# Kernel tuning notes

Hardware: AMD Instinct MI355X
Metric: run time of the kernel (lower is better)

## Reference

```python
import jax, jax.numpy as jnp
import numpy as np

DN = ('NCDHW', 'OIDHW', 'NCDHW')  # conv dimension numbers for 3D conv in torch layout
EPS = 1e-14


def setup_inputs() -> dict:
    key = jax.random.key(0)
    k1, k2 = jax.random.split(key)
    # xs: [B, C, D, H, W]
    xs = jax.random.normal(k1, (16, 128, 24, 24, 24), dtype=jnp.float32)
    # feature_vectors (prototypes): [num_features, C, w_1, h_1, L_1]
    feature_vectors = jax.random.normal(k2, (128, 128, 3, 3, 3), dtype=jnp.float32)
    return {"xs": xs, "feature_vectors": feature_vectors}


def reference(xs, feature_vectors):
    F_, C, kd, kh, kw = feature_vectors.shape
    # ||x_patch||^2: the original convolves xs**2 with all-ones weights of shape
    # [F, C, kd, kh, kw], producing F identical channels. We compute a single
    # sum-pool channel (same math) and let broadcasting supply the F channels.
    ones = jnp.ones((1, C, kd, kh, kw), dtype=xs.dtype)
    xs_squared_l2 = jax.lax.conv_general_dilated(
        xs * xs, ones, window_strides=(1, 1, 1), padding='VALID',
        dimension_numbers=DN)  # [B, 1, D', H', W']
    # ||p||^2 per prototype: [F, 1, 1, 1]
    ps_squared_l2 = jnp.sum(feature_vectors * feature_vectors,
                            axis=(1, 2, 3, 4)).reshape(-1, 1, 1, 1)
    # <x_patch, p>: the real weighted conv. [B, F, D', H', W']
    xs_conv = jax.lax.conv_general_dilated(
        xs, feature_vectors, window_strides=(1, 1, 1), padding='VALID',
        dimension_numbers=DN)
    distance = xs_squared_l2 + ps_squared_l2 - 2.0 * xs_conv
    return jnp.sqrt(jnp.abs(distance) + EPS)
```

## Files before the change

### kernel.cpp

```cpp
#include <hip/hip_runtime.h>
#include <hip/hip_bf16.h>

typedef __attribute__((ext_vector_type(8))) __bf16 bf16x8;
typedef __attribute__((ext_vector_type(2))) __bf16 bf16x2;
typedef __attribute__((ext_vector_type(4))) float f32x4;

#define B_   16
#define C_   128
#define DIM  24
#define F_   128
#define OD   22
#define OS   (OD*OD*OD)
#define SPB  (DIM*DIM*DIM)
#define K_   3456
#define M_   (B_*OS)
#define OUTN (B_*F_*OS)

__device__ __forceinline__ void async16(const void* g, void* l) {
  __builtin_amdgcn_global_load_lds(
      (const __attribute__((address_space(1))) unsigned int*)g,
      (__attribute__((address_space(3))) unsigned int*)l, 16, 0, 0);
}

__global__ __launch_bounds__(256) void prep_x(const float* __restrict__ xs,
                                              __bf16* __restrict__ xt,
                                              float* __restrict__ s1) {
  __shared__ float tile[C_ * 97];
  __shared__ float red[192];
  const int blk = blockIdx.x;
  const int yg = blk % 6;
  const int t2 = blk / 6;
  const int z = t2 % DIM;
  const int b = t2 / DIM;
  const int t = threadIdx.x;
  const float* src = xs + (size_t)b * C_ * SPB + z * (DIM * DIM) + yg * 96;
  for (int it = 0; it < 12; ++it) {
    int idx = it * 256 + t;
    int c = idx / 24, f4 = idx - c * 24;
    const float4 v = *(const float4*)(src + (size_t)c * SPB + f4 * 4);
    float* d = &tile[c * 97 + f4 * 4];
    d[0] = v.x; d[1] = v.y; d[2] = v.z; d[3] = v.w;
  }
  __syncthreads();
  size_t obase = ((size_t)b * SPB + z * (DIM * DIM) + yg * 96) * C_;
  for (int it = 0; it < 24; ++it) {
    int idx = it * 256 + t;
    int c2 = idx & 63, x = idx >> 6;
    bf16x2 v;
    v[0] = (__bf16)tile[(2 * c2) * 97 + x];
    v[1] = (__bf16)tile[(2 * c2 + 1) * 97 + x];
    *(bf16x2*)&xt[obase + (size_t)x * C_ + 2 * c2] = v;
  }
  if (t < 192) {
    int g = t / 96, p = t - g * 96;
    float s = 0.f;
    for (int c = g; c < C_; c += 2) {
      float v = tile[c * 97 + p];
      s += v * v;
    }
    red[g * 96 + p] = s;
  }
  __syncthreads();
  if (t < 96)
    s1[((size_t)b * SPB + z * (DIM * DIM) + yg * 96) + t] = red[t] + red[96 + t];
}

__global__ void prep_w(const float* __restrict__ fv, __bf16* __restrict__ Wt,
                       float* __restrict__ psq) {
  __shared__ float tile[K_];
  const int f = blockIdx.x;
  const float* src = fv + (size_t)f * K_;
  float part = 0.f;
  for (int idx = threadIdx.x; idx < K_; idx += 256) {
    float v = src[idx];
    tile[idx] = v;
    part += v * v;
  }
  __syncthreads();
  for (int idx = threadIdx.x; idx < K_; idx += 256) {
    int c = idx & 127, off = idx >> 7;
    Wt[(size_t)f * K_ + idx] = (__bf16)tile[c * 27 + off];
  }
  for (int o = 32; o > 0; o >>= 1) part += __shfl_down(part, o, 64);
  __shared__ float red[4];
  int w = threadIdx.x >> 6, l = threadIdx.x & 63;
  if (l == 0) red[w] = part;
  __syncthreads();
  if (threadIdx.x == 0) psq[f] = red[0] + red[1] + red[2] + red[3];
}

__global__ void pool_sq(const float* __restrict__ s1, float* __restrict__ xsq) {
  int i = blockIdx.x * 256 + threadIdx.x;
  if (i >= M_) return;
  int ow = i % OD;
  int t = i / OD;
  int oh = t % OD; t /= OD;
  int od = t % OD;
  int b = t / OD;
  const float* p = s1 + ((b * DIM + od) * DIM + oh) * DIM + ow;
  float s = 0.f;
#pragma unroll
  for (int dz = 0; dz < 3; ++dz)
#pragma unroll
    for (int dy = 0; dy < 3; ++dy)
#pragma unroll
      for (int dx = 0; dx < 3; ++dx)
        s += p[dz * 576 + dy * 24 + dx];
  xsq[i] = s;
}

__global__ __launch_bounds__(256) void l2gemm(
    const __bf16* __restrict__ xt, const __bf16* __restrict__ Wt,
    const float* __restrict__ xsq, const float* __restrict__ psq,
    float* __restrict__ out) {
  __shared__ __align__(16) __bf16 Wl[128 * 64];
  __shared__ __align__(16) __bf16 Pl[128 * 64];
  const int t = threadIdx.x;
  const int l = t & 63, w = t >> 6;
  const int quad = l >> 4, lan = l & 15;
  const int e = t & 7, r0 = t >> 3;
  const int esw = (e ^ (r0 & 7)) * 8;
  const int mt = blockIdx.x;

  int sb[4];
#pragma unroll
  for (int p = 0; p < 4; ++p) {
    int m = mt * 128 + r0 + 32 * p;
    int b = m / OS;
    int s = m - b * OS;
    int od = s / (OD * OD);
    int s2 = s - od * (OD * OD);
    int oh = s2 / OD;
    int ow = s2 - oh * OD;
    sb[p] = b * SPB + od * 576 + oh * 24 + ow;
  }

  f32x4 acc[4][4];
#pragma unroll
  for (int i = 0; i < 4; ++i)
#pragma unroll
    for (int n = 0; n < 4; ++n) acc[i][n] = (f32x4){0.f, 0.f, 0.f, 0.f};

  const int wm = (w >> 1) * 64;
  const int wn = (w & 1) * 64;
  __bf16* wl_base = &Wl[(w * 8) * 64];
  __bf16* pl_base = &Pl[(w * 8) * 64];

#pragma unroll 1
  for (int kt = 0; kt < 54; ++kt) {
    int off = kt >> 1;
    int dz = off / 9;
    int rem = off - dz * 9;
    int dy = rem / 3;
    int dx = rem - dy * 3;
    int doff = dz * 576 + dy * 24 + dx;
    int c0 = (kt & 1) << 6;
    __syncthreads();
#pragma unroll
    for (int p = 0; p < 4; ++p) {
      const __bf16* gp = xt + (((size_t)(sb[p] + doff)) << 7) + c0 + esw;
      async16(gp, pl_base + (size_t)(32 * p) * 64);
      const __bf16* gw = Wt + (size_t)(r0 + 32 * p) * K_ + kt * 64 + esw;
      async16(gw, wl_base + (size_t)(32 * p) * 64);
    }
    __syncthreads();
#pragma unroll
    for (int kk = 0; kk < 2; ++kk) {
      bf16x8 a[4], bb[4];
      const int swz = (((kk * 4 + quad) ^ (lan & 7))) * 8;
#pragma unroll
      for (int i = 0; i < 4; ++i)
        a[i] = *(const bf16x8*)&Wl[(wm + i * 16 + lan) * 64 + swz];
#pragma unroll
      for (int n = 0; n < 4; ++n)
        bb[n] = *(const bf16x8*)&Pl[(wn + n * 16 + lan) * 64 + swz];
#pragma unroll
      for (int i = 0; i < 4; ++i)
#pragma unroll
        for (int n = 0; n < 4; ++n)
          acc[i][n] = __builtin_amdgcn_mfma_f32_16x16x32_bf16(a[i], bb[n],
                                                              acc[i][n], 0, 0, 0);
    }
  }

  int mb[4];
  float xv[4];
#pragma unroll
  for (int n = 0; n < 4; ++n) {
    int m = mt * 128 + wn + n * 16 + lan;
    int b = m / OS;
    int s = m - b * OS;
    mb[n] = b * (F_ * OS) + s;
    xv[n] = xsq[m];
  }
#pragma unroll
  for (int i = 0; i < 4; ++i) {
#pragma unroll
    for (int r = 0; r < 4; ++r) {
      int f = wm + i * 16 + quad * 4 + r;
      float pq = psq[f];
#pragma unroll
      for (int n = 0; n < 4; ++n) {
        float d = xv[n] + pq - 2.0f * acc[i][n][r];
        out[mb[n] + f * OS] = sqrtf(fabsf(d) + 1e-14f);
      }
    }
  }
}

__global__ void l2conv_direct(const float* __restrict__ xs,
                              const float* __restrict__ fv,
                              float* __restrict__ out) {
  int i = blockIdx.x * 256 + threadIdx.x;
  if (i >= OUTN) return;
  int s = i % OS;
  int t2 = i / OS;
  int f = t2 & 127;
  int b = t2 >> 7;
  int od = s / (OD * OD);
  int s2 = s - od * (OD * OD);
  int oh = s2 / OD;
  int ow = s2 - oh * OD;
  const float* xp = xs + (size_t)b * C_ * SPB + od * 576 + oh * 24 + ow;
  const float* wp = fv + (size_t)f * K_;
  float dot = 0.f, xq = 0.f, pq = 0.f;
  for (int c = 0; c < C_; ++c) {
    const float* xpc = xp + (size_t)c * SPB;
    const float* wpc = wp + c * 27;
#pragma unroll
    for (int o = 0; o < 27; ++o) {
      int dz = o / 9;
      int ry = o - dz * 9;
      int dy = ry / 3;
      int dx = ry - dy * 3;
      float xv = xpc[dz * 576 + dy * 24 + dx];
      float wv = wpc[o];
      dot += xv * wv;
      xq += xv * xv;
      pq += wv * wv;
    }
  }
  out[i] = sqrtf(fabsf(xq + pq - 2.f * dot) + 1e-14f);
}

extern "C" void kernel_launch(void* const* d_in, const int* in_sizes, int n_in,
                              void* d_out, int out_size, void* d_ws,
                              size_t ws_size, hipStream_t stream) {
  const float* xs = (const float*)d_in[0];
  const float* fv = (const float*)d_in[1];
  float* out = (float*)d_out;

  const size_t xt_b  = (size_t)B_ * SPB * C_ * 2;
  const size_t wt_b  = (size_t)F_ * K_ * 2;
  const size_t s1_b  = (size_t)B_ * SPB * 4;
  const size_t xsq_b = (size_t)M_ * 4;
  const size_t psq_b = 512;
  if (ws_size < xt_b + wt_b + s1_b + xsq_b + psq_b) {
    l2conv_direct<<<(OUTN + 255) / 256, 256, 0, stream>>>(xs, fv, out);
    return;
  }
  char* p = (char*)d_ws;
  __bf16* xt = (__bf16*)p;          p += xt_b;
  __bf16* Wt = (__bf16*)p;          p += wt_b;
  float*  s1 = (float*)p;           p += s1_b;
  float*  xsq = (float*)p;          p += xsq_b;
  float*  psq = (float*)p;

  prep_x<<<B_ * DIM * DIM / 4, 256, 0, stream>>>(xs, xt, s1);
  prep_w<<<F_, 256, 0, stream>>>(fv, Wt, psq);
  pool_sq<<<(M_ + 255) / 256, 256, 0, stream>>>(s1, xsq);
  l2gemm<<<M_ / 128, 256, 0, stream>>>(xt, Wt, xsq, psq, out);
}
```

Measured before the change: 407.1 us.

## Double-buffer LDS tiles in l2gemm and remap blocks across XCDs

The GEMM main loop now uses two LDS buffers, issuing the async global-to-LDS loads for the next K tile before computing on the current one, with a single barrier per iteration instead of two. The goal is to overlap global load latency with MFMA work. Block indices are also remapped so that consecutive M tiles land on the same XCD, which should improve L2 reuse of the overlapping input patches. LDS use doubles to 64 KB per block, which may reduce occupancy. The loop waits only on __syncthreads, with no explicit vmcnt wait, so the compiler has to insert the correct waits for the async loads.

```diff
diff --git a/kernel.cpp b/kernel.cpp
--- a/kernel.cpp
+++ b/kernel.cpp
@@ -113,14 +113,19 @@
     const __bf16* __restrict__ xt, const __bf16* __restrict__ Wt,
     const float* __restrict__ xsq, const float* __restrict__ psq,
     float* __restrict__ out) {
-  __shared__ __align__(16) __bf16 Wl[128 * 64];
-  __shared__ __align__(16) __bf16 Pl[128 * 64];
+  __shared__ __align__(16) __bf16 Wl[2][128 * 64];
+  __shared__ __align__(16) __bf16 Pl[2][128 * 64];
   const int t = threadIdx.x;
   const int l = t & 63, w = t >> 6;
   const int quad = l >> 4, lan = l & 15;
   const int e = t & 7, r0 = t >> 3;
   const int esw = (e ^ (r0 & 7)) * 8;
-  const int mt = blockIdx.x;
+
+  const int nwg = gridDim.x;
+  const int orig = blockIdx.x;
+  const int xcd = orig & 7, lo = orig >> 3;
+  const int q = nwg >> 3, r = nwg & 7;
+  const int mt = (xcd < r ? xcd * (q + 1) : r * (q + 1) + (xcd - r) * q) + lo;
 
   int sb[4];
 #pragma unroll
@@ -143,11 +148,9 @@
 
   const int wm = (w >> 1) * 64;
   const int wn = (w & 1) * 64;
-  __bf16* wl_base = &Wl[(w * 8) * 64];
-  __bf16* pl_base = &Pl[(w * 8) * 64];
-
-#pragma unroll 1
-  for (int kt = 0; kt < 54; ++kt) {
+  const int wrow = w * 8;
+
+  auto stage = [&](int kt, int buf) {
     int off = kt >> 1;
     int dz = off / 9;
     int rem = off - dz * 9;
@@ -155,25 +158,35 @@
     int dx = rem - dy * 3;
     int doff = dz * 576 + dy * 24 + dx;
     int c0 = (kt & 1) << 6;
-    __syncthreads();
+    __bf16* wl = &Wl[buf][wrow * 64];
+    __bf16* pl = &Pl[buf][wrow * 64];
 #pragma unroll
     for (int p = 0; p < 4; ++p) {
       const __bf16* gp = xt + (((size_t)(sb[p] + doff)) << 7) + c0 + esw;
-      async16(gp, pl_base + (size_t)(32 * p) * 64);
+      async16(gp, pl + (size_t)(32 * p) * 64);
       const __bf16* gw = Wt + (size_t)(r0 + 32 * p) * K_ + kt * 64 + esw;
-      async16(gw, wl_base + (size_t)(32 * p) * 64);
-    }
-    __syncthreads();
+      async16(gw, wl + (size_t)(32 * p) * 64);
+    }
+  };
+
+  stage(0, 0);
+  __syncthreads();
+  int cur = 0;
+#pragma unroll 1
+  for (int kt = 0; kt < 54; ++kt) {
+    if (kt < 53) stage(kt + 1, cur ^ 1);
+    const __bf16* Wc = &Wl[cur][0];
+    const __bf16* Pc = &Pl[cur][0];
 #pragma unroll
     for (int kk = 0; kk < 2; ++kk) {
       bf16x8 a[4], bb[4];
       const int swz = (((kk * 4 + quad) ^ (lan & 7))) * 8;
 #pragma unroll
       for (int i = 0; i < 4; ++i)
-        a[i] = *(const bf16x8*)&Wl[(wm + i * 16 + lan) * 64 + swz];
+        a[i] = *(const bf16x8*)&Wc[(wm + i * 16 + lan) * 64 + swz];
 #pragma unroll
       for (int n = 0; n < 4; ++n)
-        bb[n] = *(const bf16x8*)&Pl[(wn + n * 16 + lan) * 64 + swz];
+        bb[n] = *(const bf16x8*)&Pc[(wn + n * 16 + lan) * 64 + swz];
 #pragma unroll
       for (int i = 0; i < 4; ++i)
 #pragma unroll
@@ -181,6 +194,8 @@
           acc[i][n] = __builtin_amdgcn_mfma_f32_16x16x32_bf16(a[i], bb[n],
                                                               acc[i][n], 0, 0, 0);
     }
+    __syncthreads();
+    cur ^= 1;
   }
 
   int mb[4];
@@ -196,12 +211,12 @@
 #pragma unroll
   for (int i = 0; i < 4; ++i) {
 #pragma unroll
-    for (int r = 0; r < 4; ++r) {
-      int f = wm + i * 16 + quad * 4 + r;
+    for (int r2 = 0; r2 < 4; ++r2) {
+      int f = wm + i * 16 + quad * 4 + r2;
       float pq = psq[f];
 #pragma unroll
       for (int n = 0; n < 4; ++n) {
-        float d = xv[n] + pq - 2.0f * acc[i][n][r];
+        float d = xv[n] + pq - 2.0f * acc[i][n][r2];
         out[mb[n] + f * OS] = sqrtf(fabsf(d) + 1e-14f);
       }
     }
```

Result: faster. 382.7 us (-6.0%).

## Enlarge GEMM M-tile to 256, remap blocks per XCD, raise MFMA priority

Applied to the files above, without the earlier changes.

The im2col GEMM now computes a 128x256 output tile per block, so each loaded weight tile is reused across twice as many patch rows. Each wave accumulates a 64x128 sub-tile in 32 accumulators, with bounds clamping for the partial last tile. Block indices are remapped so consecutive M-tiles land on the same XCD for L2 locality, and s_setprio raises wave priority around the MFMA bursts. The syncs are restructured to one before compute and one after. The cost is much higher register pressure under launch_bounds(256,2), more LDS per block, and fewer blocks in the grid.

```diff
diff --git a/kernel.cpp b/kernel.cpp
--- a/kernel.cpp
+++ b/kernel.cpp
@@ -109,23 +109,29 @@
   xsq[i] = s;
 }
 
-__global__ __launch_bounds__(256) void l2gemm(
+__global__ __launch_bounds__(256, 2) void l2gemm(
     const __bf16* __restrict__ xt, const __bf16* __restrict__ Wt,
     const float* __restrict__ xsq, const float* __restrict__ psq,
     float* __restrict__ out) {
   __shared__ __align__(16) __bf16 Wl[128 * 64];
-  __shared__ __align__(16) __bf16 Pl[128 * 64];
+  __shared__ __align__(16) __bf16 Pl[256 * 64];
   const int t = threadIdx.x;
   const int l = t & 63, w = t >> 6;
   const int quad = l >> 4, lan = l & 15;
   const int e = t & 7, r0 = t >> 3;
   const int esw = (e ^ (r0 & 7)) * 8;
-  const int mt = blockIdx.x;
-
-  int sb[4];
-#pragma unroll
-  for (int p = 0; p < 4; ++p) {
-    int m = mt * 128 + r0 + 32 * p;
+
+  const int nwg = gridDim.x;
+  const int orig = blockIdx.x;
+  const int xcd = orig & 7, lo = orig >> 3;
+  const int q = nwg >> 3, r = nwg & 7;
+  const int mt = (xcd < r ? xcd * (q + 1) : r * (q + 1) + (xcd - r) * q) + lo;
+
+  int sb[8];
+#pragma unroll
+  for (int p = 0; p < 8; ++p) {
+    int m = mt * 256 + r0 + 32 * p;
+    if (m >= M_) m = M_ - 1;
     int b = m / OS;
     int s = m - b * OS;
     int od = s / (OD * OD);
@@ -135,59 +141,66 @@
     sb[p] = b * SPB + od * 576 + oh * 24 + ow;
   }
 
-  f32x4 acc[4][4];
+  f32x4 acc[4][8];
 #pragma unroll
   for (int i = 0; i < 4; ++i)
 #pragma unroll
-    for (int n = 0; n < 4; ++n) acc[i][n] = (f32x4){0.f, 0.f, 0.f, 0.f};
-
-  const int wm = (w >> 1) * 64;
-  const int wn = (w & 1) * 64;
-  __bf16* wl_base = &Wl[(w * 8) * 64];
-  __bf16* pl_base = &Pl[(w * 8) * 64];
+    for (int n = 0; n < 8; ++n) acc[i][n] = (f32x4){0.f, 0.f, 0.f, 0.f};
+
+  const int wm = (w & 1) * 64;
+  const int wn = (w >> 1) * 128;
 
 #pragma unroll 1
   for (int kt = 0; kt < 54; ++kt) {
-    int off = kt >> 1;
-    int dz = off / 9;
-    int rem = off - dz * 9;
-    int dy = rem / 3;
-    int dx = rem - dy * 3;
-    int doff = dz * 576 + dy * 24 + dx;
-    int c0 = (kt & 1) << 6;
+    {
+      int off = kt >> 1;
+      int dz = off / 9;
+      int rem = off - dz * 9;
+      int dy = rem / 3;
+      int dx = rem - dy * 3;
+      int doff = dz * 576 + dy * 24 + dx;
+      int c0 = (kt & 1) << 6;
+#pragma unroll
+      for (int p = 0; p < 4; ++p) {
+        const __bf16* gw = Wt + (size_t)(r0 + 32 * p) * K_ + kt * 64 + esw;
+        async16(gw, &Wl[(size_t)(8 * w + 32 * p) * 64]);
+      }
+#pragma unroll
+      for (int p = 0; p < 8; ++p) {
+        const __bf16* gp = xt + (((size_t)(sb[p] + doff)) << 7) + c0 + esw;
+        async16(gp, &Pl[(size_t)(8 * w + 32 * p) * 64]);
+      }
+    }
     __syncthreads();
 #pragma unroll
-    for (int p = 0; p < 4; ++p) {
-      const __bf16* gp = xt + (((size_t)(sb[p] + doff)) << 7) + c0 + esw;
-      async16(gp, pl_base + (size_t)(32 * p) * 64);
-      const __bf16* gw = Wt + (size_t)(r0 + 32 * p) * K_ + kt * 64 + esw;
-      async16(gw, wl_base + (size_t)(32 * p) * 64);
-    }
-    __syncthreads();
-#pragma unroll
     for (int kk = 0; kk < 2; ++kk) {
-      bf16x8 a[4], bb[4];
-      const int swz = (((kk * 4 + quad) ^ (lan & 7))) * 8;
+      const int swz = ((kk * 4 + quad) ^ (lan & 7)) * 8;
+      bf16x8 a[4], bb[8];
 #pragma unroll
       for (int i = 0; i < 4; ++i)
         a[i] = *(const bf16x8*)&Wl[(wm + i * 16 + lan) * 64 + swz];
 #pragma unroll
-      for (int n = 0; n < 4; ++n)
+      for (int n = 0; n < 8; ++n)
         bb[n] = *(const bf16x8*)&Pl[(wn + n * 16 + lan) * 64 + swz];
+      __builtin_amdgcn_s_setprio(1);
 #pragma unroll
       for (int i = 0; i < 4; ++i)
 #pragma unroll
-        for (int n = 0; n < 4; ++n)
+        for (int n = 0; n < 8; ++n)
           acc[i][n] = __builtin_amdgcn_mfma_f32_16x16x32_bf16(a[i], bb[n],
                                                               acc[i][n], 0, 0, 0);
-    }
-  }
-
-  int mb[4];
-  float xv[4];
-#pragma unroll
-  for (int n = 0; n < 4; ++n) {
-    int m = mt * 128 + wn + n * 16 + lan;
+      __builtin_amdgcn_s_setprio(0);
+    }
+    __syncthreads();
+  }
+
+  int mb[8], mok[8];
+  float xv[8];
+#pragma unroll
+  for (int n = 0; n < 8; ++n) {
+    int m = mt * 256 + wn + n * 16 + lan;
+    mok[n] = (m < M_);
+    if (m >= M_) m = M_ - 1;
     int b = m / OS;
     int s = m - b * OS;
     mb[n] = b * (F_ * OS) + s;
@@ -196,13 +209,15 @@
 #pragma unroll
   for (int i = 0; i < 4; ++i) {
 #pragma unroll
-    for (int r = 0; r < 4; ++r) {
-      int f = wm + i * 16 + quad * 4 + r;
+    for (int r2 = 0; r2 < 4; ++r2) {
+      int f = wm + i * 16 + quad * 4 + r2;
       float pq = psq[f];
 #pragma unroll
-      for (int n = 0; n < 4; ++n) {
-        float d = xv[n] + pq - 2.0f * acc[i][n][r];
-        out[mb[n] + f * OS] = sqrtf(fabsf(d) + 1e-14f);
+      for (int n = 0; n < 8; ++n) {
+        if (mok[n]) {
+          float d = xv[n] + pq - 2.0f * acc[i][n][r2];
+          out[mb[n] + f * OS] = sqrtf(fabsf(d) + 1e-14f);
+        }
       }
     }
   }
@@ -269,5 +284,5 @@
   prep_x<<<B_ * DIM * DIM / 4, 256, 0, stream>>>(xs, xt, s1);
   prep_w<<<F_, 256, 0, stream>>>(fv, Wt, psq);
   pool_sq<<<(M_ + 255) / 256, 256, 0, stream>>>(s1, xsq);
-  l2gemm<<<M_ / 128, 256, 0, stream>>>(xt, Wt, xsq, psq, out);
-}
+  l2gemm<<<(M_ + 255) / 256, 256, 0, stream>>>(xt, Wt, xsq, psq, out);
+}
```

Result: no change. 414.1 us (+1.7%).
